# Kernel tuning notes

Hardware: AMD Instinct MI355X
Metric: run time of the kernel (lower is better)

The kernel has to match this reference:

```python
import jax, jax.numpy as jnp
import numpy as np

N_NODES = 50000
N_EDGES = 600000
D = 128


def sage_conv(x, edge_index, Wl, bl, Wr):
    # PyG SAGEConv (mean aggr): out = lin_l(mean_{j in N(i)} x_j) + lin_r(x_i)
    src, dst = edge_index[0], edge_index[1]
    msgs = x[src]  # [E, D] gather of neighbor features
    summed = jax.ops.segment_sum(msgs, dst, num_segments=N_NODES)  # [N, D]
    deg = jax.ops.segment_sum(jnp.ones((msgs.shape[0],), x.dtype), dst, num_segments=N_NODES)
    mean = summed / jnp.maximum(deg, 1.0)[:, None]
    return mean @ Wl.T + bl + x @ Wr.T


def setup_inputs() -> dict:
    key = jax.random.key(0)
    ks = jax.random.split(key, 12)
    s = 1.0 / np.sqrt(D)
    inp = {
        "x": jax.random.normal(ks[0], (N_NODES, D), dtype=jnp.float32),
        "edge_index": jax.random.randint(ks[1], (2, N_EDGES), 0, N_NODES, dtype=jnp.int64),
    }
    for i, layer in enumerate([1, 2, 3]):
        inp[f"Wl{layer}"] = jax.random.uniform(ks[2 + 3 * i], (D, D), jnp.float32, -s, s)
        inp[f"bl{layer}"] = jax.random.uniform(ks[3 + 3 * i], (D,), jnp.float32, -s, s)
        inp[f"Wr{layer}"] = jax.random.uniform(ks[4 + 3 * i], (D, D), jnp.float32, -s, s)
    return inp


def reference(x, edge_index, Wl1, bl1, Wr1, Wl2, bl2, Wr2, Wl3, bl3, Wr3):
    h = jax.nn.relu(sage_conv(x, edge_index, Wl1, bl1, Wr1))
    h = jax.nn.relu(sage_conv(h, edge_index, Wl2, bl2, Wr2))
    h = jax.nn.relu(sage_conv(h, edge_index, Wl3, bl3, Wr3))
    return h
```

## Files before the change

kernel.cpp:

```cpp
#include <hip/hip_runtime.h>
#include <hip/hip_bf16.h>
#include <stdint.h>

#define N_NODES 50000
#define N_EDGES 600000
#define DD 128
#define K2 256
#define M_PAD 50048
#define MAXDEG 64

typedef __bf16 bf16x8 __attribute__((ext_vector_type(8)));
typedef float floatx4 __attribute__((ext_vector_type(4)));

__device__ __forceinline__ ushort f2bf(float f) {
    union { float f; uint u; } v; v.f = f;
    uint u = v.u;
    u += 0x7fffu + ((u >> 16) & 1u);
    return (ushort)(u >> 16);
}
__device__ __forceinline__ float bf2f(ushort h) {
    union { uint u; float f; } v; v.u = ((uint)h) << 16;
    return v.f;
}


__global__ void k_cast_x(const float* __restrict__ x, ushort* __restrict__ A2,
                         int* __restrict__ cursor) {
    int idx = blockIdx.x * blockDim.x + threadIdx.x;
    if (idx < N_NODES) cursor[idx] = idx * MAXDEG;
    if (idx >= N_NODES * 64) return;
    int i = idx >> 6, l = idx & 63;
    float a = x[i * DD + 2 * l], b = x[i * DD + 2 * l + 1];
    uint p = (uint)f2bf(a) | ((uint)f2bf(b) << 16);
    *(uint*)&A2[(size_t)i * K2 + DD + 2 * l] = p;
}

__global__ void k_cast_w3(const float* __restrict__ Wl1, const float* __restrict__ Wr1,
                          const float* __restrict__ Wl2, const float* __restrict__ Wr2,
                          const float* __restrict__ Wl3, const float* __restrict__ Wr3,
                          ushort* __restrict__ Wb) {
    int idx = blockIdx.x * blockDim.x + threadIdx.x;
    if (idx >= 3 * DD * K2) return;
    int l = idx / (DD * K2);
    int r = idx - l * (DD * K2);
    int j = r >> 8, k = r & 255;
    const float* Wl = (l == 0) ? Wl1 : (l == 1) ? Wl2 : Wl3;
    const float* Wr = (l == 0) ? Wr1 : (l == 1) ? Wr2 : Wr3;
    float v = (k < DD) ? Wl[j * DD + k] : Wr[j * DD + k - DD];
    Wb[idx] = f2bf(v);
}


__global__ void k_fill(const int* __restrict__ eidx, int* __restrict__ cursor,
                       int* __restrict__ col) {
    int t = blockIdx.x * blockDim.x + threadIdx.x;
    if (t >= N_EDGES / 4) return;
    int4 s4 = ((const int4*)eidx)[t];
    int4 d4 = ((const int4*)(eidx + N_EDGES))[t];
    col[atomicAdd(&cursor[d4.x], 1)] = s4.x;
    col[atomicAdd(&cursor[d4.y], 1)] = s4.y;
    col[atomicAdd(&cursor[d4.z], 1)] = s4.z;
    col[atomicAdd(&cursor[d4.w], 1)] = s4.w;
}


__device__ __forceinline__ void accum8(float* a, uint4 p) {
    a[0] += bf2f((ushort)(p.x & 0xffffu)); a[1] += bf2f((ushort)(p.x >> 16));
    a[2] += bf2f((ushort)(p.y & 0xffffu)); a[3] += bf2f((ushort)(p.y >> 16));
    a[4] += bf2f((ushort)(p.z & 0xffffu)); a[5] += bf2f((ushort)(p.z >> 16));
    a[6] += bf2f((ushort)(p.w & 0xffffu)); a[7] += bf2f((ushort)(p.w >> 16));
}

__global__ void k_agg(ushort* __restrict__ A2,
                      const int* __restrict__ cursor, const int* __restrict__ colell) {
    int wid = (blockIdx.x * blockDim.x + threadIdx.x) >> 6;
    if (wid >= N_NODES) return;
    int lane = threadIdx.x & 63;
    int sg = lane >> 4, l16 = lane & 15;
    int s = wid * MAXDEG;
    int deg = cursor[wid] - s;
    int nb = colell[s + lane];
    float a[8] = {0, 0, 0, 0, 0, 0, 0, 0};
    const int choff = DD + l16 * 8;
    int dm1 = deg - 1;
    for (int base = 0; base < deg; base += 16) {
        int i0 = base + sg, i1 = i0 + 4, i2 = i0 + 8, i3 = i0 + 12;
        int s0 = __shfl(nb, min(i0, dm1), 64);
        int s1 = __shfl(nb, min(i1, dm1), 64);
        int s2 = __shfl(nb, min(i2, dm1), 64);
        int s3 = __shfl(nb, min(i3, dm1), 64);
        uint4 p0 = *(const uint4*)&A2[(size_t)s0 * K2 + choff];
        uint4 p1 = *(const uint4*)&A2[(size_t)s1 * K2 + choff];
        uint4 p2 = *(const uint4*)&A2[(size_t)s2 * K2 + choff];
        uint4 p3 = *(const uint4*)&A2[(size_t)s3 * K2 + choff];
        if (i0 < deg) accum8(a, p0);
        if (i1 < deg) accum8(a, p1);
        if (i2 < deg) accum8(a, p2);
        if (i3 < deg) accum8(a, p3);
    }
    float inv = 1.0f / (float)max(deg, 1);
    #pragma unroll
    for (int j = 0; j < 8; ++j) {
        float v = a[j];
        v += __shfl_xor(v, 16, 64);
        v += __shfl_xor(v, 32, 64);
        a[j] = v * inv;
    }
    if (lane < 16) {
        uint4 o;
        o.x = (uint)f2bf(a[0]) | ((uint)f2bf(a[1]) << 16);
        o.y = (uint)f2bf(a[2]) | ((uint)f2bf(a[3]) << 16);
        o.z = (uint)f2bf(a[4]) | ((uint)f2bf(a[5]) << 16);
        o.w = (uint)f2bf(a[6]) | ((uint)f2bf(a[7]) << 16);
        *(uint4*)&A2[(size_t)wid * K2 + l16 * 8] = o;
    }
}


template <bool LAST>
__global__ __launch_bounds__(256) void k_gemm(const ushort* __restrict__ A2,
                                              const ushort* __restrict__ Wb,
                                              const float* __restrict__ bias,
                                              ushort* __restrict__ A2out,
                                              float* __restrict__ out) {
    __shared__ ushort As[64 * 72];
    __shared__ ushort Bs[128 * 72];
    int tid = threadIdx.x;
    int wave = tid >> 6, lane = tid & 63;
    int quad = lane >> 4, l16 = lane & 15;
    int i0 = blockIdx.x * 64;

    floatx4 acc[8];
    for (int ct = 0; ct < 8; ++ct) acc[ct] = (floatx4){0.f, 0.f, 0.f, 0.f};

    for (int kb = 0; kb < K2; kb += 64) {
        __syncthreads();
        for (int it = 0; it < 2; ++it) {
            int idx = tid + it * 256;
            int r = idx >> 3, c = (idx & 7) * 8;
            *(uint4*)&As[r * 72 + c] =
                *(const uint4*)&A2[(size_t)(i0 + r) * K2 + kb + c];
        }
        for (int it = 0; it < 4; ++it) {
            int idx = tid + it * 256;
            int j = idx >> 3, c = (idx & 7) * 8;
            *(uint4*)&Bs[j * 72 + c] = *(const uint4*)&Wb[j * K2 + kb + c];
        }
        __syncthreads();
        for (int ks = 0; ks < 64; ks += 32) {
            bf16x8 a = *(const bf16x8*)&As[(wave * 16 + l16) * 72 + ks + quad * 8];
            for (int ct = 0; ct < 8; ++ct) {
                bf16x8 b = *(const bf16x8*)&Bs[(ct * 16 + l16) * 72 + ks + quad * 8];
                acc[ct] = __builtin_amdgcn_mfma_f32_16x16x32_bf16(a, b, acc[ct], 0, 0, 0);
            }
        }
    }
    for (int ct = 0; ct < 8; ++ct) {
        int colg = ct * 16 + l16;
        float bv = bias[colg];
        for (int r = 0; r < 4; ++r) {
            int row = i0 + wave * 16 + quad * 4 + r;
            if (row < N_NODES) {
                float v = fmaxf(acc[ct][r] + bv, 0.0f);
                if (LAST)
                    out[(size_t)row * DD + colg] = v;
                else
                    A2out[(size_t)row * K2 + DD + colg] = f2bf(v);
            }
        }
    }
}


extern "C" void kernel_launch(void* const* d_in, const int* in_sizes, int n_in,
                              void* d_out, int out_size, void* d_ws, size_t ws_size,
                              hipStream_t stream) {
    const float* x = (const float*)d_in[0];
    const int* eidx = (const int*)d_in[1];

    char* ws = (char*)d_ws;
    size_t off = 0;
    auto alloc = [&](size_t bytes) {
        void* p = ws + off;
        off += (bytes + 255) & ~(size_t)255;
        return p;
    };
    ushort* A2 = (ushort*)alloc((size_t)M_PAD * K2 * 2);
    int* cursor = (int*)alloc((size_t)N_NODES * 4);
    int* col = (int*)alloc((size_t)N_NODES * MAXDEG * 4);
    ushort* Wb = (ushort*)alloc((size_t)3 * DD * K2 * 2);
    (void)ws_size;

    k_cast_x<<<(N_NODES * 64 + 255) / 256, 256, 0, stream>>>(x, A2, cursor);
    k_cast_w3<<<(3 * DD * K2 + 255) / 256, 256, 0, stream>>>(
        (const float*)d_in[2], (const float*)d_in[4],
        (const float*)d_in[5], (const float*)d_in[7],
        (const float*)d_in[8], (const float*)d_in[10], Wb);

    k_fill<<<(N_EDGES / 4 + 255) / 256, 256, 0, stream>>>(eidx, cursor, col);

    const int aggGrid = (N_NODES * 64 + 255) / 256;
    const int gemmGrid = (N_NODES + 63) / 64;

    for (int l = 0; l < 3; ++l) {
        const float* bl = (const float*)d_in[3 + 3 * l];
        const ushort* WbL = Wb + (size_t)l * DD * K2;
        k_agg<<<aggGrid, 256, 0, stream>>>(A2, cursor, col);
        if (l < 2)
            k_gemm<false><<<gemmGrid, 256, 0, stream>>>(A2, WbL, bl, A2, nullptr);
        else
            k_gemm<true><<<gemmGrid, 256, 0, stream>>>(A2, WbL, bl, nullptr, (float*)d_out);
    }
}
```

Measured before the change: 255.1 us.

## Fuse neighbor aggregation into per-layer GEMM kernel with ping-pong feature buffers

```diff
diff --git a/kernel.cpp b/kernel.cpp
--- a/kernel.cpp
+++ b/kernel.cpp
@@ -22,32 +22,43 @@
     union { uint u; float f; } v; v.u = ((uint)h) << 16;
     return v.f;
 }
-
-
-__global__ void k_cast_x(const float* __restrict__ x, ushort* __restrict__ A2,
-                         int* __restrict__ cursor) {
+__device__ __forceinline__ void accum8(float* a, uint4 p) {
+    a[0] += bf2f((ushort)(p.x & 0xffffu)); a[1] += bf2f((ushort)(p.x >> 16));
+    a[2] += bf2f((ushort)(p.y & 0xffffu)); a[3] += bf2f((ushort)(p.y >> 16));
+    a[4] += bf2f((ushort)(p.z & 0xffffu)); a[5] += bf2f((ushort)(p.z >> 16));
+    a[6] += bf2f((ushort)(p.w & 0xffffu)); a[7] += bf2f((ushort)(p.w >> 16));
+}
+__device__ __forceinline__ uint4 pack8(const float* a, float s) {
+    uint4 o;
+    o.x = (uint)f2bf(a[0] * s) | ((uint)f2bf(a[1] * s) << 16);
+    o.y = (uint)f2bf(a[2] * s) | ((uint)f2bf(a[3] * s) << 16);
+    o.z = (uint)f2bf(a[4] * s) | ((uint)f2bf(a[5] * s) << 16);
+    o.w = (uint)f2bf(a[6] * s) | ((uint)f2bf(a[7] * s) << 16);
+    return o;
+}
+
+
+__global__ void k_prep(const float* __restrict__ x, ushort* __restrict__ X0,
+                       int* __restrict__ cursor,
+                       const float* __restrict__ Wl1, const float* __restrict__ Wr1,
+                       const float* __restrict__ Wl2, const float* __restrict__ Wr2,
+                       const float* __restrict__ Wl3, const float* __restrict__ Wr3,
+                       ushort* __restrict__ Wb) {
     int idx = blockIdx.x * blockDim.x + threadIdx.x;
-    if (idx < N_NODES) cursor[idx] = idx * MAXDEG;
+    if (idx < M_PAD) cursor[idx] = idx * MAXDEG;
+    if (idx < 3 * DD * K2) {
+        int l = idx / (DD * K2);
+        int r = idx - l * (DD * K2);
+        int j = r >> 8, k = r & 255;
+        const float* Wl = (l == 0) ? Wl1 : (l == 1) ? Wl2 : Wl3;
+        const float* Wr = (l == 0) ? Wr1 : (l == 1) ? Wr2 : Wr3;
+        float v = (k < DD) ? Wl[j * DD + k] : Wr[j * DD + k - DD];
+        Wb[idx] = f2bf(v);
+    }
     if (idx >= N_NODES * 64) return;
     int i = idx >> 6, l = idx & 63;
     float a = x[i * DD + 2 * l], b = x[i * DD + 2 * l + 1];
-    uint p = (uint)f2bf(a) | ((uint)f2bf(b) << 16);
-    *(uint*)&A2[(size_t)i * K2 + DD + 2 * l] = p;
-}
-
-__global__ void k_cast_w3(const float* __restrict__ Wl1, const float* __restrict__ Wr1,
-                          const float* __restrict__ Wl2, const float* __restrict__ Wr2,
-                          const float* __restrict__ Wl3, const float* __restrict__ Wr3,
-                          ushort* __restrict__ Wb) {
-    int idx = blockIdx.x * blockDim.x + threadIdx.x;
-    if (idx >= 3 * DD * K2) return;
-    int l = idx / (DD * K2);
-    int r = idx - l * (DD * K2);
-    int j = r >> 8, k = r & 255;
-    const float* Wl = (l == 0) ? Wl1 : (l == 1) ? Wl2 : Wl3;
-    const float* Wr = (l == 0) ? Wr1 : (l == 1) ? Wr2 : Wr3;
-    float v = (k < DD) ? Wl[j * DD + k] : Wr[j * DD + k - DD];
-    Wb[idx] = f2bf(v);
+    *(uint*)&X0[(size_t)i * DD + 2 * l] = (uint)f2bf(a) | ((uint)f2bf(b) << 16);
 }
 
 
@@ -64,83 +75,65 @@
 }
 
 
-__device__ __forceinline__ void accum8(float* a, uint4 p) {
-    a[0] += bf2f((ushort)(p.x & 0xffffu)); a[1] += bf2f((ushort)(p.x >> 16));
-    a[2] += bf2f((ushort)(p.y & 0xffffu)); a[3] += bf2f((ushort)(p.y >> 16));
-    a[4] += bf2f((ushort)(p.z & 0xffffu)); a[5] += bf2f((ushort)(p.z >> 16));
-    a[6] += bf2f((ushort)(p.w & 0xffffu)); a[7] += bf2f((ushort)(p.w >> 16));
-}
-
-__global__ void k_agg(ushort* __restrict__ A2,
-                      const int* __restrict__ cursor, const int* __restrict__ colell) {
-    int wid = (blockIdx.x * blockDim.x + threadIdx.x) >> 6;
-    if (wid >= N_NODES) return;
-    int lane = threadIdx.x & 63;
-    int sg = lane >> 4, l16 = lane & 15;
-    int s = wid * MAXDEG;
-    int deg = cursor[wid] - s;
-    int nb = colell[s + lane];
-    float a[8] = {0, 0, 0, 0, 0, 0, 0, 0};
-    const int choff = DD + l16 * 8;
-    int dm1 = deg - 1;
-    for (int base = 0; base < deg; base += 16) {
-        int i0 = base + sg, i1 = i0 + 4, i2 = i0 + 8, i3 = i0 + 12;
-        int s0 = __shfl(nb, min(i0, dm1), 64);
-        int s1 = __shfl(nb, min(i1, dm1), 64);
-        int s2 = __shfl(nb, min(i2, dm1), 64);
-        int s3 = __shfl(nb, min(i3, dm1), 64);
-        uint4 p0 = *(const uint4*)&A2[(size_t)s0 * K2 + choff];
-        uint4 p1 = *(const uint4*)&A2[(size_t)s1 * K2 + choff];
-        uint4 p2 = *(const uint4*)&A2[(size_t)s2 * K2 + choff];
-        uint4 p3 = *(const uint4*)&A2[(size_t)s3 * K2 + choff];
-        if (i0 < deg) accum8(a, p0);
-        if (i1 < deg) accum8(a, p1);
-        if (i2 < deg) accum8(a, p2);
-        if (i3 < deg) accum8(a, p3);
-    }
-    float inv = 1.0f / (float)max(deg, 1);
-    #pragma unroll
-    for (int j = 0; j < 8; ++j) {
-        float v = a[j];
-        v += __shfl_xor(v, 16, 64);
-        v += __shfl_xor(v, 32, 64);
-        a[j] = v * inv;
-    }
-    if (lane < 16) {
-        uint4 o;
-        o.x = (uint)f2bf(a[0]) | ((uint)f2bf(a[1]) << 16);
-        o.y = (uint)f2bf(a[2]) | ((uint)f2bf(a[3]) << 16);
-        o.z = (uint)f2bf(a[4]) | ((uint)f2bf(a[5]) << 16);
-        o.w = (uint)f2bf(a[6]) | ((uint)f2bf(a[7]) << 16);
-        *(uint4*)&A2[(size_t)wid * K2 + l16 * 8] = o;
-    }
-}
-
-
 template <bool LAST>
-__global__ __launch_bounds__(256) void k_gemm(const ushort* __restrict__ A2,
-                                              const ushort* __restrict__ Wb,
-                                              const float* __restrict__ bias,
-                                              ushort* __restrict__ A2out,
-                                              float* __restrict__ out) {
-    __shared__ ushort As[64 * 72];
+__global__ __launch_bounds__(256, 3) void k_layer(
+    const ushort* __restrict__ Xin, const int* __restrict__ cursor,
+    const int* __restrict__ colell, const ushort* __restrict__ Wb,
+    const float* __restrict__ bias, ushort* __restrict__ Xout,
+    float* __restrict__ out) {
+    __shared__ ushort As[64 * 264];
     __shared__ ushort Bs[128 * 72];
     int tid = threadIdx.x;
     int wave = tid >> 6, lane = tid & 63;
+    int i0 = blockIdx.x * 64;
+
+    {
+        int l8 = lane & 7, sg = lane >> 3;
+        int nbase = i0 + wave * 16;
+        for (int n = 0; n < 16; ++n) {
+            int node = nbase + n;
+            int deg = cursor[node] - node * MAXDEG;
+            int nb = colell[node * MAXDEG + lane];
+            float a[16];
+            #pragma unroll
+            for (int j = 0; j < 16; ++j) a[j] = 0.f;
+            int dm1 = deg - 1;
+            for (int base = 0; base < deg; base += 8) {
+                int idx = base + sg;
+                int src = __shfl(nb, min(idx, dm1), 64);
+                const ushort* row = Xin + (size_t)src * DD;
+                uint4 p0 = *(const uint4*)&row[l8 * 8];
+                uint4 p1 = *(const uint4*)&row[(l8 + 8) * 8];
+                if (idx < deg) { accum8(a, p0); accum8(a + 8, p1); }
+            }
+            #pragma unroll
+            for (int j = 0; j < 16; ++j) {
+                float v = a[j];
+                v += __shfl_xor(v, 8, 64);
+                v += __shfl_xor(v, 16, 64);
+                v += __shfl_xor(v, 32, 64);
+                a[j] = v;
+            }
+            float inv = 1.0f / (float)max(deg, 1);
+            if (lane < 8) {
+                *(uint4*)&As[(wave * 16 + n) * 264 + l8 * 8] = pack8(a, inv);
+                *(uint4*)&As[(wave * 16 + n) * 264 + (l8 + 8) * 8] = pack8(a + 8, inv);
+            }
+        }
+    }
+    for (int it = 0; it < 4; ++it) {
+        int idx = tid + it * 256;
+        int r = idx >> 4, c = (idx & 15) * 8;
+        *(uint4*)&As[r * 264 + DD + c] = *(const uint4*)&Xin[(size_t)(i0 + r) * DD + c];
+    }
+
     int quad = lane >> 4, l16 = lane & 15;
-    int i0 = blockIdx.x * 64;
-
     floatx4 acc[8];
+    #pragma unroll
     for (int ct = 0; ct < 8; ++ct) acc[ct] = (floatx4){0.f, 0.f, 0.f, 0.f};
 
     for (int kb = 0; kb < K2; kb += 64) {
         __syncthreads();
-        for (int it = 0; it < 2; ++it) {
-            int idx = tid + it * 256;
-            int r = idx >> 3, c = (idx & 7) * 8;
-            *(uint4*)&As[r * 72 + c] =
-                *(const uint4*)&A2[(size_t)(i0 + r) * K2 + kb + c];
-        }
         for (int it = 0; it < 4; ++it) {
             int idx = tid + it * 256;
             int j = idx >> 3, c = (idx & 7) * 8;
@@ -148,16 +141,20 @@
         }
         __syncthreads();
         for (int ks = 0; ks < 64; ks += 32) {
-            bf16x8 a = *(const bf16x8*)&As[(wave * 16 + l16) * 72 + ks + quad * 8];
+            bf16x8 a = *(const bf16x8*)&As[(wave * 16 + l16) * 264 + kb + ks + quad * 8];
+            #pragma unroll
             for (int ct = 0; ct < 8; ++ct) {
                 bf16x8 b = *(const bf16x8*)&Bs[(ct * 16 + l16) * 72 + ks + quad * 8];
                 acc[ct] = __builtin_amdgcn_mfma_f32_16x16x32_bf16(a, b, acc[ct], 0, 0, 0);
             }
         }
     }
+
+    #pragma unroll
     for (int ct = 0; ct < 8; ++ct) {
         int colg = ct * 16 + l16;
         float bv = bias[colg];
+        #pragma unroll
         for (int r = 0; r < 4; ++r) {
             int row = i0 + wave * 16 + quad * 4 + r;
             if (row < N_NODES) {
@@ -165,7 +162,7 @@
                 if (LAST)
                     out[(size_t)row * DD + colg] = v;
                 else
-                    A2out[(size_t)row * K2 + DD + colg] = f2bf(v);
+                    Xout[(size_t)row * DD + colg] = f2bf(v);
             }
         }
     }
@@ -185,30 +182,27 @@
         off += (bytes + 255) & ~(size_t)255;
         return p;
     };
-    ushort* A2 = (ushort*)alloc((size_t)M_PAD * K2 * 2);
-    int* cursor = (int*)alloc((size_t)N_NODES * 4);
-    int* col = (int*)alloc((size_t)N_NODES * MAXDEG * 4);
+    ushort* X0 = (ushort*)alloc((size_t)M_PAD * DD * 2);
+    ushort* X1 = (ushort*)alloc((size_t)M_PAD * DD * 2);
+    int* cursor = (int*)alloc((size_t)M_PAD * 4);
+    int* col = (int*)alloc((size_t)M_PAD * MAXDEG * 4);
     ushort* Wb = (ushort*)alloc((size_t)3 * DD * K2 * 2);
     (void)ws_size;
 
-    k_cast_x<<<(N_NODES * 64 + 255) / 256, 256, 0, stream>>>(x, A2, cursor);
-    k_cast_w3<<<(3 * DD * K2 + 255) / 256, 256, 0, stream>>>(
+    k_prep<<<(N_NODES * 64 + 255) / 256, 256, 0, stream>>>(
+        x, X0, cursor,
         (const float*)d_in[2], (const float*)d_in[4],
         (const float*)d_in[5], (const float*)d_in[7],
         (const float*)d_in[8], (const float*)d_in[10], Wb);
 
     k_fill<<<(N_EDGES / 4 + 255) / 256, 256, 0, stream>>>(eidx, cursor, col);
 
-    const int aggGrid = (N_NODES * 64 + 255) / 256;
-    const int gemmGrid = (N_NODES + 63) / 64;
-
-    for (int l = 0; l < 3; ++l) {
-        const float* bl = (const float*)d_in[3 + 3 * l];
-        const ushort* WbL = Wb + (size_t)l * DD * K2;
-        k_agg<<<aggGrid, 256, 0, stream>>>(A2, cursor, col);
-        if (l < 2)
-            k_gemm<false><<<gemmGrid, 256, 0, stream>>>(A2, WbL, bl, A2, nullptr);
-        else
-            k_gemm<true><<<gemmGrid, 256, 0, stream>>>(A2, WbL, bl, nullptr, (float*)d_out);
-    }
-}
+    const int grid = M_PAD / 64;
+
+    k_layer<false><<<grid, 256, 0, stream>>>(X0, cursor, col, Wb,
+        (const float*)d_in[3], X1, nullptr);
+    k_layer<false><<<grid, 256, 0, stream>>>(X1, cursor, col, Wb + (size_t)DD * K2,
+        (const float*)d_in[6], X0, nullptr);
+    k_layer<true><<<grid, 256, 0, stream>>>(X0, cursor, col, Wb + (size_t)2 * DD * K2,
+        (const float*)d_in[9], nullptr, (float*)d_out);
+}
```

Measured after the change: 379.2 us. +48.6%, slower.

## Fuse all phases into one persistent cooperative kernel with grid syncs

Applied to the files above, without the earlier changes.

```diff
diff --git a/kernel.cpp b/kernel.cpp
--- a/kernel.cpp
+++ b/kernel.cpp
@@ -1,6 +1,9 @@
 #include <hip/hip_runtime.h>
+#include <hip/hip_cooperative_groups.h>
 #include <hip/hip_bf16.h>
 #include <stdint.h>
+
+namespace cg = cooperative_groups;
 
 #define N_NODES 50000
 #define N_EDGES 600000
@@ -8,6 +11,7 @@
 #define K2 256
 #define M_PAD 50048
 #define MAXDEG 64
+#define NTILES (M_PAD / 64)
 
 typedef __bf16 bf16x8 __attribute__((ext_vector_type(8)));
 typedef float floatx4 __attribute__((ext_vector_type(4)));
@@ -22,48 +26,6 @@
     union { uint u; float f; } v; v.u = ((uint)h) << 16;
     return v.f;
 }
-
-
-__global__ void k_cast_x(const float* __restrict__ x, ushort* __restrict__ A2,
-                         int* __restrict__ cursor) {
-    int idx = blockIdx.x * blockDim.x + threadIdx.x;
-    if (idx < N_NODES) cursor[idx] = idx * MAXDEG;
-    if (idx >= N_NODES * 64) return;
-    int i = idx >> 6, l = idx & 63;
-    float a = x[i * DD + 2 * l], b = x[i * DD + 2 * l + 1];
-    uint p = (uint)f2bf(a) | ((uint)f2bf(b) << 16);
-    *(uint*)&A2[(size_t)i * K2 + DD + 2 * l] = p;
-}
-
-__global__ void k_cast_w3(const float* __restrict__ Wl1, const float* __restrict__ Wr1,
-                          const float* __restrict__ Wl2, const float* __restrict__ Wr2,
-                          const float* __restrict__ Wl3, const float* __restrict__ Wr3,
-                          ushort* __restrict__ Wb) {
-    int idx = blockIdx.x * blockDim.x + threadIdx.x;
-    if (idx >= 3 * DD * K2) return;
-    int l = idx / (DD * K2);
-    int r = idx - l * (DD * K2);
-    int j = r >> 8, k = r & 255;
-    const float* Wl = (l == 0) ? Wl1 : (l == 1) ? Wl2 : Wl3;
-    const float* Wr = (l == 0) ? Wr1 : (l == 1) ? Wr2 : Wr3;
-    float v = (k < DD) ? Wl[j * DD + k] : Wr[j * DD + k - DD];
-    Wb[idx] = f2bf(v);
-}
-
-
-__global__ void k_fill(const int* __restrict__ eidx, int* __restrict__ cursor,
-                       int* __restrict__ col) {
-    int t = blockIdx.x * blockDim.x + threadIdx.x;
-    if (t >= N_EDGES / 4) return;
-    int4 s4 = ((const int4*)eidx)[t];
-    int4 d4 = ((const int4*)(eidx + N_EDGES))[t];
-    col[atomicAdd(&cursor[d4.x], 1)] = s4.x;
-    col[atomicAdd(&cursor[d4.y], 1)] = s4.y;
-    col[atomicAdd(&cursor[d4.z], 1)] = s4.z;
-    col[atomicAdd(&cursor[d4.w], 1)] = s4.w;
-}
-
-
 __device__ __forceinline__ void accum8(float* a, uint4 p) {
     a[0] += bf2f((ushort)(p.x & 0xffffu)); a[1] += bf2f((ushort)(p.x >> 16));
     a[2] += bf2f((ushort)(p.y & 0xffffu)); a[3] += bf2f((ushort)(p.y >> 16));
@@ -71,113 +33,189 @@
     a[6] += bf2f((ushort)(p.w & 0xffffu)); a[7] += bf2f((ushort)(p.w >> 16));
 }
 
-__global__ void k_agg(ushort* __restrict__ A2,
-                      const int* __restrict__ cursor, const int* __restrict__ colell) {
-    int wid = (blockIdx.x * blockDim.x + threadIdx.x) >> 6;
-    if (wid >= N_NODES) return;
+struct Params {
+    const float* x;
+    const int* eidx;
+    const float* W[6];
+    const float* b[3];
+    ushort* A2;
+    int* cursor;
+    int* col;
+    ushort* Wb;
+    float* out;
+};
+
+
+__device__ void prep_phase(const Params& p, int gtid, int stride) {
+    for (int idx = gtid; idx < N_NODES * 64; idx += stride) {
+        if (idx < M_PAD) p.cursor[idx] = idx * MAXDEG;
+        if (idx < 3 * DD * K2) {
+            int l = idx / (DD * K2);
+            int r = idx - l * (DD * K2);
+            int j = r >> 8, k = r & 255;
+            const float* Wl = p.W[2 * l];
+            const float* Wr = p.W[2 * l + 1];
+            float v = (k < DD) ? Wl[j * DD + k] : Wr[j * DD + k - DD];
+            p.Wb[idx] = f2bf(v);
+        }
+        int i = idx >> 6, l2 = idx & 63;
+        float a = p.x[(size_t)i * DD + 2 * l2], b = p.x[(size_t)i * DD + 2 * l2 + 1];
+        *(uint*)&p.A2[(size_t)i * K2 + DD + 2 * l2] =
+            (uint)f2bf(a) | ((uint)f2bf(b) << 16);
+    }
+}
+
+__device__ void fill_phase(const Params& p, int gtid, int stride) {
+    for (int t = gtid; t < N_EDGES / 4; t += stride) {
+        int4 s4 = ((const int4*)p.eidx)[t];
+        int4 d4 = ((const int4*)(p.eidx + N_EDGES))[t];
+        p.col[atomicAdd(&p.cursor[d4.x], 1)] = s4.x;
+        p.col[atomicAdd(&p.cursor[d4.y], 1)] = s4.y;
+        p.col[atomicAdd(&p.cursor[d4.z], 1)] = s4.z;
+        p.col[atomicAdd(&p.cursor[d4.w], 1)] = s4.w;
+    }
+}
+
+__device__ void agg_phase(ushort* __restrict__ A2, const int* __restrict__ cursor,
+                          const int* __restrict__ colell, int gwave, int nwaves) {
     int lane = threadIdx.x & 63;
     int sg = lane >> 4, l16 = lane & 15;
-    int s = wid * MAXDEG;
-    int deg = cursor[wid] - s;
-    int nb = colell[s + lane];
-    float a[8] = {0, 0, 0, 0, 0, 0, 0, 0};
     const int choff = DD + l16 * 8;
-    int dm1 = deg - 1;
-    for (int base = 0; base < deg; base += 16) {
-        int i0 = base + sg, i1 = i0 + 4, i2 = i0 + 8, i3 = i0 + 12;
-        int s0 = __shfl(nb, min(i0, dm1), 64);
-        int s1 = __shfl(nb, min(i1, dm1), 64);
-        int s2 = __shfl(nb, min(i2, dm1), 64);
-        int s3 = __shfl(nb, min(i3, dm1), 64);
-        uint4 p0 = *(const uint4*)&A2[(size_t)s0 * K2 + choff];
-        uint4 p1 = *(const uint4*)&A2[(size_t)s1 * K2 + choff];
-        uint4 p2 = *(const uint4*)&A2[(size_t)s2 * K2 + choff];
-        uint4 p3 = *(const uint4*)&A2[(size_t)s3 * K2 + choff];
-        if (i0 < deg) accum8(a, p0);
-        if (i1 < deg) accum8(a, p1);
-        if (i2 < deg) accum8(a, p2);
-        if (i3 < deg) accum8(a, p3);
-    }
-    float inv = 1.0f / (float)max(deg, 1);
-    #pragma unroll
-    for (int j = 0; j < 8; ++j) {
-        float v = a[j];
-        v += __shfl_xor(v, 16, 64);
-        v += __shfl_xor(v, 32, 64);
-        a[j] = v * inv;
-    }
-    if (lane < 16) {
-        uint4 o;
-        o.x = (uint)f2bf(a[0]) | ((uint)f2bf(a[1]) << 16);
-        o.y = (uint)f2bf(a[2]) | ((uint)f2bf(a[3]) << 16);
-        o.z = (uint)f2bf(a[4]) | ((uint)f2bf(a[5]) << 16);
-        o.w = (uint)f2bf(a[6]) | ((uint)f2bf(a[7]) << 16);
-        *(uint4*)&A2[(size_t)wid * K2 + l16 * 8] = o;
-    }
-}
-
-
-template <bool LAST>
-__global__ __launch_bounds__(256) void k_gemm(const ushort* __restrict__ A2,
-                                              const ushort* __restrict__ Wb,
-                                              const float* __restrict__ bias,
-                                              ushort* __restrict__ A2out,
-                                              float* __restrict__ out) {
-    __shared__ ushort As[64 * 72];
-    __shared__ ushort Bs[128 * 72];
+    for (int wid = gwave; wid < N_NODES; wid += nwaves) {
+        int s = wid * MAXDEG;
+        int deg = cursor[wid] - s;
+        int nb = colell[s + lane];
+        float a[8] = {0, 0, 0, 0, 0, 0, 0, 0};
+        int dm1 = deg - 1;
+        for (int base = 0; base < deg; base += 16) {
+            int i0 = base + sg, i1 = i0 + 4, i2 = i0 + 8, i3 = i0 + 12;
+            int s0 = __shfl(nb, min(i0, dm1), 64);
+            int s1 = __shfl(nb, min(i1, dm1), 64);
+            int s2 = __shfl(nb, min(i2, dm1), 64);
+            int s3 = __shfl(nb, min(i3, dm1), 64);
+            uint4 p0 = *(const uint4*)&A2[(size_t)s0 * K2 + choff];
+            uint4 p1 = *(const uint4*)&A2[(size_t)s1 * K2 + choff];
+            uint4 p2 = *(const uint4*)&A2[(size_t)s2 * K2 + choff];
+            uint4 p3 = *(const uint4*)&A2[(size_t)s3 * K2 + choff];
+            if (i0 < deg) accum8(a, p0);
+            if (i1 < deg) accum8(a, p1);
+            if (i2 < deg) accum8(a, p2);
+            if (i3 < deg) accum8(a, p3);
+        }
+        float inv = 1.0f / (float)max(deg, 1);
+        #pragma unroll
+        for (int j = 0; j < 8; ++j) {
+            float v = a[j];
+            v += __shfl_xor(v, 16, 64);
+            v += __shfl_xor(v, 32, 64);
+            a[j] = v * inv;
+        }
+        if (lane < 16) {
+            uint4 o;
+            o.x = (uint)f2bf(a[0]) | ((uint)f2bf(a[1]) << 16);
+            o.y = (uint)f2bf(a[2]) | ((uint)f2bf(a[3]) << 16);
+            o.z = (uint)f2bf(a[4]) | ((uint)f2bf(a[5]) << 16);
+            o.w = (uint)f2bf(a[6]) | ((uint)f2bf(a[7]) << 16);
+            *(uint4*)&A2[(size_t)wid * K2 + l16 * 8] = o;
+        }
+    }
+}
+
+__device__ void gemm_phase(ushort* As, ushort* Bs, ushort* __restrict__ A2,
+                           const ushort* __restrict__ Wb, const float* __restrict__ bias,
+                           float* __restrict__ out, bool last, int tile0, int tstride) {
     int tid = threadIdx.x;
     int wave = tid >> 6, lane = tid & 63;
     int quad = lane >> 4, l16 = lane & 15;
-    int i0 = blockIdx.x * 64;
-
-    floatx4 acc[8];
-    for (int ct = 0; ct < 8; ++ct) acc[ct] = (floatx4){0.f, 0.f, 0.f, 0.f};
-
-    for (int kb = 0; kb < K2; kb += 64) {
-        __syncthreads();
-        for (int it = 0; it < 2; ++it) {
-            int idx = tid + it * 256;
-            int r = idx >> 3, c = (idx & 7) * 8;
-            *(uint4*)&As[r * 72 + c] =
-                *(const uint4*)&A2[(size_t)(i0 + r) * K2 + kb + c];
-        }
-        for (int it = 0; it < 4; ++it) {
-            int idx = tid + it * 256;
-            int j = idx >> 3, c = (idx & 7) * 8;
-            *(uint4*)&Bs[j * 72 + c] = *(const uint4*)&Wb[j * K2 + kb + c];
-        }
-        __syncthreads();
-        for (int ks = 0; ks < 64; ks += 32) {
-            bf16x8 a = *(const bf16x8*)&As[(wave * 16 + l16) * 72 + ks + quad * 8];
-            for (int ct = 0; ct < 8; ++ct) {
-                bf16x8 b = *(const bf16x8*)&Bs[(ct * 16 + l16) * 72 + ks + quad * 8];
-                acc[ct] = __builtin_amdgcn_mfma_f32_16x16x32_bf16(a, b, acc[ct], 0, 0, 0);
-            }
-        }
-    }
-    for (int ct = 0; ct < 8; ++ct) {
-        int colg = ct * 16 + l16;
-        float bv = bias[colg];
-        for (int r = 0; r < 4; ++r) {
-            int row = i0 + wave * 16 + quad * 4 + r;
-            if (row < N_NODES) {
-                float v = fmaxf(acc[ct][r] + bv, 0.0f);
-                if (LAST)
-                    out[(size_t)row * DD + colg] = v;
-                else
-                    A2out[(size_t)row * K2 + DD + colg] = f2bf(v);
-            }
-        }
-    }
+    for (int tile = tile0; tile < NTILES; tile += tstride) {
+        int i0 = tile * 64;
+        floatx4 acc[8];
+        #pragma unroll
+        for (int ct = 0; ct < 8; ++ct) acc[ct] = (floatx4){0.f, 0.f, 0.f, 0.f};
+
+        for (int kb = 0; kb < K2; kb += 64) {
+            __syncthreads();
+            for (int it = 0; it < 2; ++it) {
+                int idx = tid + it * 256;
+                int r = idx >> 3, c = (idx & 7) * 8;
+                *(uint4*)&As[r * 72 + c] =
+                    *(const uint4*)&A2[(size_t)(i0 + r) * K2 + kb + c];
+            }
+            for (int it = 0; it < 4; ++it) {
+                int idx = tid + it * 256;
+                int j = idx >> 3, c = (idx & 7) * 8;
+                *(uint4*)&Bs[j * 72 + c] = *(const uint4*)&Wb[j * K2 + kb + c];
+            }
+            __syncthreads();
+            for (int ks = 0; ks < 64; ks += 32) {
+                bf16x8 a = *(const bf16x8*)&As[(wave * 16 + l16) * 72 + ks + quad * 8];
+                #pragma unroll
+                for (int ct = 0; ct < 8; ++ct) {
+                    bf16x8 b = *(const bf16x8*)&Bs[(ct * 16 + l16) * 72 + ks + quad * 8];
+                    acc[ct] = __builtin_amdgcn_mfma_f32_16x16x32_bf16(a, b, acc[ct], 0, 0, 0);
+                }
+            }
+        }
+        #pragma unroll
+        for (int ct = 0; ct < 8; ++ct) {
+            int colg = ct * 16 + l16;
+            float bv = bias[colg];
+            #pragma unroll
+            for (int r = 0; r < 4; ++r) {
+                int row = i0 + wave * 16 + quad * 4 + r;
+                if (row < N_NODES) {
+                    float v = fmaxf(acc[ct][r] + bv, 0.0f);
+                    if (last)
+                        out[(size_t)row * DD + colg] = v;
+                    else
+                        A2[(size_t)row * K2 + DD + colg] = f2bf(v);
+                }
+            }
+        }
+    }
+}
+
+__global__ __launch_bounds__(256, 4) void k_mega(Params p) {
+    __shared__ ushort As[64 * 72];
+    __shared__ ushort Bs[128 * 72];
+    cg::grid_group grid = cg::this_grid();
+    int nb = gridDim.x;
+    int gtid = blockIdx.x * 256 + threadIdx.x;
+    int stride = nb * 256;
+
+    prep_phase(p, gtid, stride);
+    grid.sync();
+    fill_phase(p, gtid, stride);
+    for (int layer = 0; layer < 3; ++layer) {
+        grid.sync();
+        agg_phase(p.A2, p.cursor, p.col, blockIdx.x * 4 + (threadIdx.x >> 6), nb * 4);
+        grid.sync();
+        gemm_phase(As, Bs, p.A2, p.Wb + (size_t)layer * DD * K2,
+                   p.b[layer], p.out, layer == 2, blockIdx.x, nb);
+    }
+}
+
+__global__ void k_prep_g(Params p) {
+    prep_phase(p, blockIdx.x * blockDim.x + threadIdx.x, gridDim.x * blockDim.x);
+}
+__global__ void k_fill_g(Params p) {
+    fill_phase(p, blockIdx.x * blockDim.x + threadIdx.x, gridDim.x * blockDim.x);
+}
+__global__ void k_agg_g(Params p) {
+    agg_phase(p.A2, p.cursor, p.col,
+              blockIdx.x * 4 + (threadIdx.x >> 6), gridDim.x * 4);
+}
+__global__ __launch_bounds__(256) void k_gemm_g(Params p, int layer) {
+    __shared__ ushort As[64 * 72];
+    __shared__ ushort Bs[128 * 72];
+    gemm_phase(As, Bs, p.A2, p.Wb + (size_t)layer * DD * K2,
+               p.b[layer], p.out, layer == 2, blockIdx.x, gridDim.x);
 }
 
 
 extern "C" void kernel_launch(void* const* d_in, const int* in_sizes, int n_in,
                               void* d_out, int out_size, void* d_ws, size_t ws_size,
                               hipStream_t stream) {
-    const float* x = (const float*)d_in[0];
-    const int* eidx = (const int*)d_in[1];
-
     char* ws = (char*)d_ws;
     size_t off = 0;
     auto alloc = [&](size_t bytes) {
@@ -185,30 +223,40 @@
         off += (bytes + 255) & ~(size_t)255;
         return p;
     };
-    ushort* A2 = (ushort*)alloc((size_t)M_PAD * K2 * 2);
-    int* cursor = (int*)alloc((size_t)N_NODES * 4);
-    int* col = (int*)alloc((size_t)N_NODES * MAXDEG * 4);
-    ushort* Wb = (ushort*)alloc((size_t)3 * DD * K2 * 2);
+    Params p;
+    p.x = (const float*)d_in[0];
+    p.eidx = (const int*)d_in[1];
+    p.W[0] = (const float*)d_in[2];  p.W[1] = (const float*)d_in[4];
+    p.W[2] = (const float*)d_in[5];  p.W[3] = (const float*)d_in[7];
+    p.W[4] = (const float*)d_in[8];  p.W[5] = (const float*)d_in[10];
+    p.b[0] = (const float*)d_in[3];
+    p.b[1] = (const float*)d_in[6];
+    p.b[2] = (const float*)d_in[9];
+    p.A2 = (ushort*)alloc((size_t)M_PAD * K2 * 2);
+    p.cursor = (int*)alloc((size_t)M_PAD * 4);
+    p.col = (int*)alloc((size_t)M_PAD * MAXDEG * 4);
+    p.Wb = (ushort*)alloc((size_t)3 * DD * K2 * 2);
+    p.out = (float*)d_out;
     (void)ws_size;
 
-    k_cast_x<<<(N_NODES * 64 + 255) / 256, 256, 0, stream>>>(x, A2, cursor);
-    k_cast_w3<<<(3 * DD * K2 + 255) / 256, 256, 0, stream>>>(
-        (const float*)d_in[2], (const float*)d_in[4],
-        (const float*)d_in[5], (const float*)d_in[7],
-        (const float*)d_in[8], (const float*)d_in[10], Wb);
-
-    k_fill<<<(N_EDGES / 4 + 255) / 256, 256, 0, stream>>>(eidx, cursor, col);
-
-    const int aggGrid = (N_NODES * 64 + 255) / 256;
-    const int gemmGrid = (N_NODES + 63) / 64;
-
-    for (int l = 0; l < 3; ++l) {
-        const float* bl = (const float*)d_in[3 + 3 * l];
-        const ushort* WbL = Wb + (size_t)l * DD * K2;
-        k_agg<<<aggGrid, 256, 0, stream>>>(A2, cursor, col);
-        if (l < 2)
-            k_gemm<false><<<gemmGrid, 256, 0, stream>>>(A2, WbL, bl, A2, nullptr);
-        else
-            k_gemm<true><<<gemmGrid, 256, 0, stream>>>(A2, WbL, bl, nullptr, (float*)d_out);
-    }
-}
+    bool coop_ok = false;
+    int maxB = 0;
+    if (hipOccupancyMaxActiveBlocksPerMultiprocessor(&maxB, k_mega, 256, 0) == hipSuccess
+        && maxB > 0) {
+        int grid = maxB * 256;
+        if (grid > 1024) grid = 1024;
+        void* args[] = {&p};
+        if (hipLaunchCooperativeKernel((const void*)k_mega, dim3(grid), dim3(256),
+                                       args, 0, stream) == hipSuccess)
+            coop_ok = true;
+    }
+    if (!coop_ok) {
+        k_prep_g<<<(N_NODES * 64 + 255) / 256, 256, 0, stream>>>(p);
+        k_fill_g<<<(N_EDGES / 4 + 255) / 256, 256, 0, stream>>>(p);
+        const int aggGrid = (N_NODES + 3) / 4;
+        for (int l = 0; l < 3; ++l) {
+            k_agg_g<<<aggGrid, 256, 0, stream>>>(p);
+            k_gemm_g<<<NTILES, 256, 0, stream>>>(p, l);
+        }
+    }
+}
```

Result: slower. 296.7 us (+16.3%).
